# Optimization experiments

Hardware: AMD Instinct MI355X
Metric: run time of the kernel (lower is better)

The kernel has to match this reference:

```python
import jax, jax.numpy as jnp
import numpy as np

B, T, C = 2, 8192, 1024
H, BS, LW = 16, 64, 128          # num_heads, block_size, local_window_size
D = C // H                        # head_dim = 64
W = BS + LW                       # max window length per block = 192
NB = T // BS                      # number of blocks


def setup_inputs() -> dict:
    key = jax.random.key(0)
    ks = jax.random.split(key, 11)
    s = 1.0 / np.sqrt(C)          # small init so softmax is not saturated
    return {
        'query': jax.random.normal(ks[0], (B, T, C), jnp.float32),
        'key':   jax.random.normal(ks[1], (B, T, C), jnp.float32),
        'value': jax.random.normal(ks[2], (B, T, C), jnp.float32),
        'Wq': jax.random.normal(ks[3], (C, C), jnp.float32) * s,
        'bq': jax.random.normal(ks[4], (C,), jnp.float32) * s,
        'Wk': jax.random.normal(ks[5], (C, C), jnp.float32) * s,
        'bk': jax.random.normal(ks[6], (C,), jnp.float32) * s,
        'Wv': jax.random.normal(ks[7], (C, C), jnp.float32) * s,
        'bv': jax.random.normal(ks[8], (C,), jnp.float32) * s,
        'Wo': jax.random.normal(ks[9], (C, C), jnp.float32) * s,
        'bo': jax.random.normal(ks[10], (C,), jnp.float32) * s,
    }


def reference(query, key, value, Wq, bq, Wk, bk, Wv, bv, Wo, bo):
    # projections -> (B, H, T, D)
    def proj(x, Wt, bt):
        return (x @ Wt.T + bt).reshape(B, T, H, D).transpose(0, 2, 1, 3)

    scale = jnp.asarray(D, query.dtype) ** -0.5
    q = proj(query, Wq, bq) * scale
    k = proj(key, Wk, bk)
    v = proj(value, Wv, bv)

    # per-block window indices: block i attends to [i - LW//2, i + BS + LW//2)
    starts = jnp.arange(NB) * BS                              # (NB,)
    idx = starts[:, None] + jnp.arange(-LW // 2, BS + LW // 2)  # (NB, W)
    valid = (idx >= 0) & (idx < T)                            # (NB, W)
    cidx = jnp.clip(idx, 0, T - 1)

    q_blk = q.reshape(B, H, NB, BS, D)
    k_win = k[:, :, cidx, :]                                  # (B, H, NB, W, D)
    v_win = v[:, :, cidx, :]

    scores = jnp.einsum('bhnqd,bhnkd->bhnqk', q_blk, k_win).astype(jnp.float32)
    scores = jnp.where(valid[None, None, :, None, :], scores, -jnp.inf)
    probs = jax.nn.softmax(scores, axis=-1).astype(q.dtype)

    out = jnp.einsum('bhnqk,bhnkd->bhnqd', probs, v_win)      # (B, H, NB, BS, D)
    out = out.reshape(B, H, T, D).transpose(0, 2, 1, 3).reshape(B, T, C)
    return out @ Wo.T + bo
```

## Files before the change

### kernel.cpp

```cpp
#include <hip/hip_runtime.h>
#include <hip/hip_bf16.h>
#include <type_traits>

#define BATCH 2
#define SEQ   8192
#define CH    1024
#define NH    16
#define BLK   64
#define WIN   192
#define NBL   128
#define DH    64
#define MR    (BATCH*SEQ)

typedef __bf16 bf16x8 __attribute__((ext_vector_type(8)));
typedef float  f32x4  __attribute__((ext_vector_type(4)));

__device__ __forceinline__ f32x4 zero4() {
    f32x4 z; z[0]=0.f; z[1]=0.f; z[2]=0.f; z[3]=0.f; return z;
}

union Pack8 { __hip_bfloat16 h[8]; uint4 u; };

typedef const __attribute__((address_space(1))) unsigned int* gas_ptr;
typedef       __attribute__((address_space(3))) unsigned int* las_ptr;

__device__ __forceinline__ void gload_lds16(const __hip_bfloat16* g, __hip_bfloat16* l) {
    __builtin_amdgcn_global_load_lds((gas_ptr)(const void*)g, (las_ptr)(void*)l, 16, 0, 0);
}

__device__ __forceinline__ int xcd_swz(int bid, int nwg) {
    return (bid & 7) * (nwg >> 3) + (bid >> 3);
}

__global__ __launch_bounds__(256) void pack_bf16(
    const float* __restrict__ src, __hip_bfloat16* __restrict__ dst, int n8)
{
    int i = blockIdx.x * 256 + threadIdx.x;
    if (i >= n8) return;
    const float4* s = reinterpret_cast<const float4*>(src);
    float4 a = s[2 * i], b = s[2 * i + 1];
    Pack8 p;
    p.h[0] = __float2bfloat16(a.x); p.h[1] = __float2bfloat16(a.y);
    p.h[2] = __float2bfloat16(a.z); p.h[3] = __float2bfloat16(a.w);
    p.h[4] = __float2bfloat16(b.x); p.h[5] = __float2bfloat16(b.y);
    p.h[6] = __float2bfloat16(b.z); p.h[7] = __float2bfloat16(b.w);
    reinterpret_cast<uint4*>(dst)[i] = p.u;
}


__device__ __forceinline__ void stage_half(
    const __hip_bfloat16* __restrict__ g, int goff,
    __hip_bfloat16* sm, int loff, int tid)
{
    gload_lds16(g + goff,            sm + loff + tid * 8);
    gload_lds16(g + goff + 128 * CH, sm + loff + (tid + 512) * 8);
}

template<int MH, int KS>
__device__ __forceinline__ void phase_mfma(
    const __hip_bfloat16* As_, const __hip_bfloat16* Bs_,
    int aoff, int boff, f32x4 (&acc)[8][4])
{
    bf16x8 af[4], bf[4];
    #pragma unroll
    for (int i = 0; i < 4; ++i)
        af[i] = *reinterpret_cast<const bf16x8*>(As_ + KS * 8192 + (MH * 4 + i) * 512 + aoff);
    #pragma unroll
    for (int j = 0; j < 4; ++j)
        bf[j] = *reinterpret_cast<const bf16x8*>(Bs_ + KS * 8192 + j * 512 + boff);
    asm volatile("s_waitcnt lgkmcnt(0)" ::: "memory");
    __builtin_amdgcn_sched_barrier(0);
    __builtin_amdgcn_s_setprio(1);
    #pragma unroll
    for (int i = 0; i < 4; ++i)
        #pragma unroll
        for (int j = 0; j < 4; ++j)
            acc[MH * 4 + i][j] = __builtin_amdgcn_mfma_f32_16x16x32_bf16(
                af[i], bf[j], acc[MH * 4 + i][j], 0, 0, 0);
    __builtin_amdgcn_s_setprio(0);
}

template<typename OT>
__device__ __forceinline__ void gemm_body256(
    const __hip_bfloat16* __restrict__ A, const __hip_bfloat16* __restrict__ Wb,
    const float* __restrict__ bias, OT* __restrict__ out, float alpha,
    int m0, int n0, __hip_bfloat16* sm)
{
    const int tid  = threadIdx.x;
    const int wid  = tid >> 6;
    const int lane = tid & 63;
    const int quad = lane >> 4;
    const int l16  = lane & 15;
    const int wr   = wid >> 2, wc = wid & 3;

    const int r0 = tid >> 2;
    const int s0 = (tid & 3) ^ (r0 & 3);
    const int offA0 = (m0 + r0) * CH + s0 * 8;
    const int offB0 = (n0 + r0) * CH + s0 * 8;

    const int cq   = quad ^ (l16 & 3);
    const int aoff = ((wr * 128 + l16) * 4 + cq) * 8;
    const int boff = ((wc * 64  + l16) * 4 + cq) * 8;

    f32x4 acc[8][4];
    #pragma unroll
    for (int i = 0; i < 8; ++i)
        #pragma unroll
        for (int j = 0; j < 4; ++j) acc[i][j] = zero4();

    stage_half(A,  offA0,      sm, 0,             tid);
    stage_half(Wb, offB0,      sm, 32768,         tid);
    stage_half(A,  offA0 + 32, sm, 8192,          tid);
    stage_half(Wb, offB0 + 32, sm, 32768 + 8192,  tid);

    #pragma unroll 1
    for (int t = 0; t < 15; ++t) {
        const int cur = t & 1, nb = cur ^ 1;
        const int kn  = (t + 1) * 64;
        const __hip_bfloat16* As_ = sm + cur * 16384;
        const __hip_bfloat16* Bs_ = sm + 32768 + cur * 16384;

        asm volatile("s_waitcnt vmcnt(4)" ::: "memory");
        __builtin_amdgcn_s_barrier();
        __builtin_amdgcn_sched_barrier(0);
        stage_half(A, offA0 + kn, sm, nb * 16384, tid);
        phase_mfma<0, 0>(As_, Bs_, aoff, boff, acc);

        __builtin_amdgcn_s_barrier();
        __builtin_amdgcn_sched_barrier(0);
        stage_half(Wb, offB0 + kn, sm, 32768 + nb * 16384, tid);
        phase_mfma<1, 0>(As_, Bs_, aoff, boff, acc);

        asm volatile("s_waitcnt vmcnt(4)" ::: "memory");
        __builtin_amdgcn_s_barrier();
        __builtin_amdgcn_sched_barrier(0);
        stage_half(A, offA0 + kn + 32, sm, nb * 16384 + 8192, tid);
        phase_mfma<0, 1>(As_, Bs_, aoff, boff, acc);

        __builtin_amdgcn_s_barrier();
        __builtin_amdgcn_sched_barrier(0);
        stage_half(Wb, offB0 + kn + 32, sm, 32768 + nb * 16384 + 8192, tid);
        phase_mfma<1, 1>(As_, Bs_, aoff, boff, acc);
    }

    {
        const __hip_bfloat16* As_ = sm + 16384;
        const __hip_bfloat16* Bs_ = sm + 32768 + 16384;

        asm volatile("s_waitcnt vmcnt(4)" ::: "memory");
        __builtin_amdgcn_s_barrier();
        __builtin_amdgcn_sched_barrier(0);
        phase_mfma<0, 0>(As_, Bs_, aoff, boff, acc);

        __builtin_amdgcn_s_barrier();
        __builtin_amdgcn_sched_barrier(0);
        phase_mfma<1, 0>(As_, Bs_, aoff, boff, acc);

        asm volatile("s_waitcnt vmcnt(0)" ::: "memory");
        __builtin_amdgcn_s_barrier();
        __builtin_amdgcn_sched_barrier(0);
        phase_mfma<0, 1>(As_, Bs_, aoff, boff, acc);

        __builtin_amdgcn_s_barrier();
        __builtin_amdgcn_sched_barrier(0);
        phase_mfma<1, 1>(As_, Bs_, aoff, boff, acc);
    }

    #pragma unroll
    for (int j = 0; j < 4; ++j) {
        const int col = n0 + wc * 64 + j * 16 + l16;
        const float bv = bias[col];
        #pragma unroll
        for (int i = 0; i < 8; ++i) {
            #pragma unroll
            for (int r = 0; r < 4; ++r) {
                const int row = m0 + wr * 128 + i * 16 + quad * 4 + r;
                float v = alpha * (acc[i][j][r] + bv);
                if constexpr (std::is_same<OT, float>::value)
                    out[(size_t)row * CH + col] = v;
                else
                    out[(size_t)row * CH + col] = __float2bfloat16(v);
            }
        }
    }
}

__device__ __forceinline__ void gemm_tile256(int& m0, int& n0) {
    int bid = blockIdx.y * 4 + blockIdx.x;
    int swz = (bid & 7) * 32 + (bid >> 3);
    m0 = (swz >> 2) * 256;
    n0 = (swz & 3) * 256;
}

__global__ __launch_bounds__(512, 2) void gemm_qk256(
    const __hip_bfloat16* __restrict__ A0, const __hip_bfloat16* __restrict__ W0,
    const float* __restrict__ b0, __hip_bfloat16* __restrict__ o0, float alpha0,
    const __hip_bfloat16* __restrict__ A1, const __hip_bfloat16* __restrict__ W1,
    const float* __restrict__ b1, __hip_bfloat16* __restrict__ o1)
{
    __shared__ alignas(16) __hip_bfloat16 sm[65536];
    int m0, n0; gemm_tile256(m0, n0);
    if (blockIdx.z == 0)
        gemm_body256<__hip_bfloat16>(A0, W0, b0, o0, alpha0, m0, n0, sm);
    else
        gemm_body256<__hip_bfloat16>(A1, W1, b1, o1, 1.0f, m0, n0, sm);
}

template<typename OT>
__global__ __launch_bounds__(512, 2) void gemm_one256(
    const __hip_bfloat16* __restrict__ A, const __hip_bfloat16* __restrict__ Wb,
    const float* __restrict__ bias, OT* __restrict__ out)
{
    __shared__ alignas(16) __hip_bfloat16 sm[65536];
    int m0, n0; gemm_tile256(m0, n0);
    gemm_body256<OT>(A, Wb, bias, out, 1.0f, m0, n0, sm);
}

__global__ __launch_bounds__(256) void attn_kernel(
    const __hip_bfloat16* __restrict__ qg,
    const __hip_bfloat16* __restrict__ kg,
    const __hip_bfloat16* __restrict__ vg,
    __hip_bfloat16* __restrict__ ctx)
{
    __shared__ alignas(16) char smem[62464];
    auto qs = reinterpret_cast<__hip_bfloat16(*)[72]>(smem);
    auto ks = reinterpret_cast<__hip_bfloat16(*)[72]>(smem + 9216);
    auto vt = reinterpret_cast<__hip_bfloat16(*)[200]>(smem + 36864);
    auto ps = reinterpret_cast<__hip_bfloat16(*)[200]>(smem);

    const int blk = xcd_swz(blockIdx.x, BATCH * NH * NBL);
    const int n = blk & (NBL - 1);
    const int h = (blk >> 7) & (NH - 1);
    const int b = blk >> 11;
    const int t0  = n * BLK;
    const int kst = t0 - 64;
    const int tid = threadIdx.x;
    const size_t baseBH = (size_t)b * SEQ * CH + (size_t)h * DH;

    #pragma unroll
    for (int it = 0; it < 2; it++) {
        int c = tid + it * 256;
        int row = c >> 3, seg = c & 7;
        *reinterpret_cast<uint4*>(&qs[row][seg * 8]) =
            *reinterpret_cast<const uint4*>(qg + baseBH + (size_t)(t0 + row) * CH + seg * 8);
    }
    #pragma unroll
    for (int it = 0; it < 6; it++) {
        int c = tid + it * 256;
        int row = c >> 3, seg = c & 7;
        int tr = kst + row; tr = tr < 0 ? 0 : (tr >= SEQ ? SEQ - 1 : tr);
        *reinterpret_cast<uint4*>(&ks[row][seg * 8]) =
            *reinterpret_cast<const uint4*>(kg + baseBH + (size_t)tr * CH + seg * 8);
    }
    #pragma unroll
    for (int it = 0; it < 6; it++) {
        int c = tid + it * 256;
        int j = c % WIN, seg = c / WIN;
        int tr = kst + j; tr = tr < 0 ? 0 : (tr >= SEQ ? SEQ - 1 : tr);
        Pack8 p;
        p.u = *reinterpret_cast<const uint4*>(vg + baseBH + (size_t)tr * CH + seg * 8);
        #pragma unroll
        for (int e = 0; e < 8; e++) vt[seg * 8 + e][j] = p.h[e];
    }
    __syncthreads();

    const int wid = tid >> 6, lane = tid & 63, quad = lane >> 4, l16 = lane & 15;

    f32x4 sc[12];
    #pragma unroll
    for (int j = 0; j < 12; j++) sc[j] = zero4();
    #pragma unroll
    for (int kk = 0; kk < 2; kk++) {
        bf16x8 aq = *reinterpret_cast<const bf16x8*>(&qs[wid * 16 + l16][kk * 32 + quad * 8]);
        #pragma unroll
        for (int j = 0; j < 12; j++) {
            bf16x8 bk = *reinterpret_cast<const bf16x8*>(&ks[j * 16 + l16][kk * 32 + quad * 8]);
            sc[j] = __builtin_amdgcn_mfma_f32_16x16x32_bf16(aq, bk, sc[j], 0, 0, 0);
        }
    }
    __syncthreads();

    #pragma unroll
    for (int r = 0; r < 4; r++) {
        float s[12];
        float mx = -3.0e38f;
        #pragma unroll
        for (int j = 0; j < 12; j++) {
            int col = j * 16 + l16;
            int tr = kst + col;
            bool valid = (tr >= 0) && (tr < SEQ);
            s[j] = valid ? sc[j][r] : -3.0e38f;
            mx = fmaxf(mx, s[j]);
        }
        #pragma unroll
        for (int o = 1; o < 16; o <<= 1) mx = fmaxf(mx, __shfl_xor(mx, o, 64));
        float sum = 0.f;
        #pragma unroll
        for (int j = 0; j < 12; j++) {
            float e = __expf(s[j] - mx);
            s[j] = e;
            sum += e;
        }
        #pragma unroll
        for (int o = 1; o < 16; o <<= 1) sum += __shfl_xor(sum, o, 64);
        const float inv = 1.f / sum;
        const int row = wid * 16 + quad * 4 + r;
        #pragma unroll
        for (int j = 0; j < 12; j++)
            ps[row][j * 16 + l16] = __float2bfloat16(s[j] * inv);
    }
    __syncthreads();

    f32x4 oa[4];
    #pragma unroll
    for (int j = 0; j < 4; j++) oa[j] = zero4();
    #pragma unroll
    for (int kk = 0; kk < 6; kk++) {
        bf16x8 ap = *reinterpret_cast<const bf16x8*>(&ps[wid * 16 + l16][kk * 32 + quad * 8]);
        #pragma unroll
        for (int j = 0; j < 4; j++) {
            bf16x8 bv = *reinterpret_cast<const bf16x8*>(&vt[j * 16 + l16][kk * 32 + quad * 8]);
            oa[j] = __builtin_amdgcn_mfma_f32_16x16x32_bf16(ap, bv, oa[j], 0, 0, 0);
        }
    }
    #pragma unroll
    for (int j = 0; j < 4; j++) {
        const int d = j * 16 + l16;
        #pragma unroll
        for (int r = 0; r < 4; r++) {
            const int i = wid * 16 + quad * 4 + r;
            ctx[baseBH + (size_t)(t0 + i) * CH + d] = __float2bfloat16(oa[j][r]);
        }
    }
}

extern "C" void kernel_launch(void* const* d_in, const int* in_sizes, int n_in,
                              void* d_out, int out_size, void* d_ws, size_t ws_size,
                              hipStream_t stream)
{
    const float* query = (const float*)d_in[0];
    const float* key_i = (const float*)d_in[1];
    const float* value = (const float*)d_in[2];
    const float* Wq = (const float*)d_in[3];
    const float* bq = (const float*)d_in[4];
    const float* Wk = (const float*)d_in[5];
    const float* bk = (const float*)d_in[6];
    const float* Wv = (const float*)d_in[7];
    const float* bv = (const float*)d_in[8];
    const float* Wo = (const float*)d_in[9];
    const float* bo = (const float*)d_in[10];
    float* out = (float*)d_out;

    const size_t NELEM = (size_t)MR * CH;
    const size_t WELEM = (size_t)CH * CH;

    __hip_bfloat16* S0 = (__hip_bfloat16*)d_ws;
    __hip_bfloat16* S1 = S0 + NELEM;
    __hip_bfloat16* S2 = S1 + NELEM;
    __hip_bfloat16* S3 = S2 + NELEM;
    __hip_bfloat16* wqb = S3;
    __hip_bfloat16* wkb = S3 + WELEM;
    __hip_bfloat16* wvb = S3 + 2 * WELEM;
    __hip_bfloat16* wob = S3 + 3 * WELEM;

    __hip_bfloat16* xq = (__hip_bfloat16*)d_out;
    __hip_bfloat16* xk = xq + NELEM;
    __hip_bfloat16* vb = (__hip_bfloat16*)d_out;
    __hip_bfloat16* qb = S1;
    __hip_bfloat16* kb = S2;
    __hip_bfloat16* cb = S0;

    const int nA8 = (int)(NELEM / 8);
    const int nW8 = (int)(WELEM / 8);

    pack_bf16<<<nA8 / 256, 256, 0, stream>>>(query, xq, nA8);
    pack_bf16<<<nA8 / 256, 256, 0, stream>>>(key_i, xk, nA8);
    pack_bf16<<<nA8 / 256, 256, 0, stream>>>(value, S0, nA8);
    pack_bf16<<<nW8 / 256, 256, 0, stream>>>(Wq, wqb, nW8);
    pack_bf16<<<nW8 / 256, 256, 0, stream>>>(Wk, wkb, nW8);
    pack_bf16<<<nW8 / 256, 256, 0, stream>>>(Wv, wvb, nW8);
    pack_bf16<<<nW8 / 256, 256, 0, stream>>>(Wo, wob, nW8);

    dim3 ggrid(CH / 256, MR / 256);
    dim3 qkgrid(CH / 256, MR / 256, 2);

    gemm_qk256<<<qkgrid, 512, 0, stream>>>(xq, wqb, bq, qb, 0.125f,
                                           xk, wkb, bk, kb);
    gemm_one256<__hip_bfloat16><<<ggrid, 512, 0, stream>>>(S0, wvb, bv, vb);

    attn_kernel<<<BATCH * NH * NBL, 256, 0, stream>>>(qb, kb, vb, cb);

    gemm_one256<float><<<ggrid, 512, 0, stream>>>(cb, wob, bo, out);
}
```

Baseline: 451.8 us.

## Merge GEMM phases, interleave LDS fragment loads with MFMAs, change LDS swizzle

The projection GEMM's four half-phases per K-step become two. Each phase now issues both the A and B global-to-LDS loads, then runs all 8x4 MFMAs, which halves the number of workgroup barriers. Within a phase, A fragments are loaded from LDS in a rolling fashion with partial lgkmcnt waits, so MFMAs start before every fragment arrives. The LDS XOR swizzle now uses row bits 1-2 instead of bits 0-1, to reduce bank conflicts on fragment reads. This adds register pressure from keeping all B fragments plus rotating A fragments live, and issues the loads in larger bursts.

```diff
diff --git a/kernel.cpp b/kernel.cpp
--- a/kernel.cpp
+++ b/kernel.cpp
@@ -56,27 +56,44 @@
     gload_lds16(g + goff + 128 * CH, sm + loff + (tid + 512) * 8);
 }
 
-template<int MH, int KS>
-__device__ __forceinline__ void phase_mfma(
+#define SB0 __builtin_amdgcn_sched_barrier(0)
+#define LGKM(n) do { asm volatile("s_waitcnt lgkmcnt(" #n ")" ::: "memory"); \
+                     __builtin_amdgcn_sched_barrier(0); } while (0)
+#define MFMA4(i, areg) do { \
+    acc[i][0] = __builtin_amdgcn_mfma_f32_16x16x32_bf16(areg, bf0, acc[i][0], 0, 0, 0); \
+    acc[i][1] = __builtin_amdgcn_mfma_f32_16x16x32_bf16(areg, bf1, acc[i][1], 0, 0, 0); \
+    acc[i][2] = __builtin_amdgcn_mfma_f32_16x16x32_bf16(areg, bf2, acc[i][2], 0, 0, 0); \
+    acc[i][3] = __builtin_amdgcn_mfma_f32_16x16x32_bf16(areg, bf3, acc[i][3], 0, 0, 0); } while (0)
+
+template<int KS>
+__device__ __forceinline__ void phase_mfma2(
     const __hip_bfloat16* As_, const __hip_bfloat16* Bs_,
     int aoff, int boff, f32x4 (&acc)[8][4])
 {
-    bf16x8 af[4], bf[4];
-    #pragma unroll
-    for (int i = 0; i < 4; ++i)
-        af[i] = *reinterpret_cast<const bf16x8*>(As_ + KS * 8192 + (MH * 4 + i) * 512 + aoff);
-    #pragma unroll
-    for (int j = 0; j < 4; ++j)
-        bf[j] = *reinterpret_cast<const bf16x8*>(Bs_ + KS * 8192 + j * 512 + boff);
-    asm volatile("s_waitcnt lgkmcnt(0)" ::: "memory");
-    __builtin_amdgcn_sched_barrier(0);
+    const __hip_bfloat16* Ak = As_ + KS * 8192;
+    const __hip_bfloat16* Bk = Bs_ + KS * 8192;
+    bf16x8 bf0 = *reinterpret_cast<const bf16x8*>(Bk + boff);
+    bf16x8 bf1 = *reinterpret_cast<const bf16x8*>(Bk + boff + 512);
+    bf16x8 bf2 = *reinterpret_cast<const bf16x8*>(Bk + boff + 1024);
+    bf16x8 bf3 = *reinterpret_cast<const bf16x8*>(Bk + boff + 1536);
+    bf16x8 a0  = *reinterpret_cast<const bf16x8*>(Ak + aoff);
+    bf16x8 a1  = *reinterpret_cast<const bf16x8*>(Ak + aoff + 512);
+    bf16x8 a2  = *reinterpret_cast<const bf16x8*>(Ak + aoff + 1024);
+    SB0;
     __builtin_amdgcn_s_setprio(1);
-    #pragma unroll
-    for (int i = 0; i < 4; ++i)
-        #pragma unroll
-        for (int j = 0; j < 4; ++j)
-            acc[MH * 4 + i][j] = __builtin_amdgcn_mfma_f32_16x16x32_bf16(
-                af[i], bf[j], acc[MH * 4 + i][j], 0, 0, 0);
+    LGKM(2);  MFMA4(0, a0);
+    bf16x8 a3 = *reinterpret_cast<const bf16x8*>(Ak + aoff + 3 * 512); SB0;
+    LGKM(2);  MFMA4(1, a1);
+    a0 = *reinterpret_cast<const bf16x8*>(Ak + aoff + 4 * 512); SB0;
+    LGKM(2);  MFMA4(2, a2);
+    a1 = *reinterpret_cast<const bf16x8*>(Ak + aoff + 5 * 512); SB0;
+    LGKM(2);  MFMA4(3, a3);
+    a2 = *reinterpret_cast<const bf16x8*>(Ak + aoff + 6 * 512); SB0;
+    LGKM(2);  MFMA4(4, a0);
+    a3 = *reinterpret_cast<const bf16x8*>(Ak + aoff + 7 * 512); SB0;
+    LGKM(2);  MFMA4(5, a1);
+    LGKM(1);  MFMA4(6, a2);
+    LGKM(0);  MFMA4(7, a3);
     __builtin_amdgcn_s_setprio(0);
 }
 
@@ -94,11 +111,11 @@
     const int wr   = wid >> 2, wc = wid & 3;
 
     const int r0 = tid >> 2;
-    const int s0 = (tid & 3) ^ (r0 & 3);
+    const int s0 = (tid & 3) ^ ((tid >> 3) & 3);
     const int offA0 = (m0 + r0) * CH + s0 * 8;
     const int offB0 = (n0 + r0) * CH + s0 * 8;
 
-    const int cq   = quad ^ (l16 & 3);
+    const int cq   = quad ^ ((l16 >> 1) & 3);
     const int aoff = ((wr * 128 + l16) * 4 + cq) * 8;
     const int boff = ((wc * 64  + l16) * 4 + cq) * 8;
 
@@ -122,25 +139,17 @@
 
         asm volatile("s_waitcnt vmcnt(4)" ::: "memory");
         __builtin_amdgcn_s_barrier();
-        __builtin_amdgcn_sched_barrier(0);
-        stage_half(A, offA0 + kn, sm, nb * 16384, tid);
-        phase_mfma<0, 0>(As_, Bs_, aoff, boff, acc);
-
-        __builtin_amdgcn_s_barrier();
-        __builtin_amdgcn_sched_barrier(0);
+        SB0;
+        stage_half(A,  offA0 + kn, sm, nb * 16384, tid);
         stage_half(Wb, offB0 + kn, sm, 32768 + nb * 16384, tid);
-        phase_mfma<1, 0>(As_, Bs_, aoff, boff, acc);
+        phase_mfma2<0>(As_, Bs_, aoff, boff, acc);
 
         asm volatile("s_waitcnt vmcnt(4)" ::: "memory");
         __builtin_amdgcn_s_barrier();
-        __builtin_amdgcn_sched_barrier(0);
-        stage_half(A, offA0 + kn + 32, sm, nb * 16384 + 8192, tid);
-        phase_mfma<0, 1>(As_, Bs_, aoff, boff, acc);
-
-        __builtin_amdgcn_s_barrier();
-        __builtin_amdgcn_sched_barrier(0);
+        SB0;
+        stage_half(A,  offA0 + kn + 32, sm, nb * 16384 + 8192, tid);
         stage_half(Wb, offB0 + kn + 32, sm, 32768 + nb * 16384 + 8192, tid);
-        phase_mfma<1, 1>(As_, Bs_, aoff, boff, acc);
+        phase_mfma2<1>(As_, Bs_, aoff, boff, acc);
     }
 
     {
@@ -149,21 +158,13 @@
 
         asm volatile("s_waitcnt vmcnt(4)" ::: "memory");
         __builtin_amdgcn_s_barrier();
-        __builtin_amdgcn_sched_barrier(0);
-        phase_mfma<0, 0>(As_, Bs_, aoff, boff, acc);
-
-        __builtin_amdgcn_s_barrier();
-        __builtin_amdgcn_sched_barrier(0);
-        phase_mfma<1, 0>(As_, Bs_, aoff, boff, acc);
+        SB0;
+        phase_mfma2<0>(As_, Bs_, aoff, boff, acc);
 
         asm volatile("s_waitcnt vmcnt(0)" ::: "memory");
         __builtin_amdgcn_s_barrier();
-        __builtin_amdgcn_sched_barrier(0);
-        phase_mfma<0, 1>(As_, Bs_, aoff, boff, acc);
-
-        __builtin_amdgcn_s_barrier();
-        __builtin_amdgcn_sched_barrier(0);
-        phase_mfma<1, 1>(As_, Bs_, aoff, boff, acc);
+        SB0;
+        phase_mfma2<1>(As_, Bs_, aoff, boff, acc);
     }
 
     #pragma unroll
```

Result: no change. 447.6 us (-0.9%).

## Reorder GEMM LDS reads before global stages, reuse B fragments, change LDS swizzle

Applied to the files above, without the earlier changes.

Restructures the 256-tile GEMM main loop so each phase issues its LDS fragment reads before the next global-to-LDS stage, then waits at a barrier and runs the MFMAs. B fragments are loaded once per K-slice and reused across both M halves, which cuts redundant LDS reads. The XOR swizzle now uses bits 1-2 of the row instead of bits 0-1, aimed at fewer LDS bank conflicts. The barrier and vmcnt placement changes the hazard ordering between LDS reads and async writes, which could cost correctness or add stalls if the ordering is wrong.

```diff
diff --git a/kernel.cpp b/kernel.cpp
--- a/kernel.cpp
+++ b/kernel.cpp
@@ -56,27 +56,38 @@
     gload_lds16(g + goff + 128 * CH, sm + loff + (tid + 512) * 8);
 }
 
-template<int MH, int KS>
-__device__ __forceinline__ void phase_mfma(
-    const __hip_bfloat16* As_, const __hip_bfloat16* Bs_,
-    int aoff, int boff, f32x4 (&acc)[8][4])
-{
-    bf16x8 af[4], bf[4];
+#define SB0 __builtin_amdgcn_sched_barrier(0)
+#define LGKM0 do { asm volatile("s_waitcnt lgkmcnt(0)" ::: "memory"); \
+                   __builtin_amdgcn_sched_barrier(0); } while (0)
+#define VMCNT(n) do { asm volatile("s_waitcnt vmcnt(" #n ")" ::: "memory"); \
+                      __builtin_amdgcn_sched_barrier(0); } while (0)
+
+template<int MH, bool RB>
+__device__ __forceinline__ void phase_reads(
+    const __hip_bfloat16* Ak, const __hip_bfloat16* Bk,
+    int aoff, int boff, bf16x8 (&af)[4], bf16x8 (&bfk)[4])
+{
+    if constexpr (RB) {
+        #pragma unroll
+        for (int j = 0; j < 4; ++j)
+            bfk[j] = *reinterpret_cast<const bf16x8*>(Bk + boff + j * 512);
+    }
     #pragma unroll
     for (int i = 0; i < 4; ++i)
-        af[i] = *reinterpret_cast<const bf16x8*>(As_ + KS * 8192 + (MH * 4 + i) * 512 + aoff);
-    #pragma unroll
-    for (int j = 0; j < 4; ++j)
-        bf[j] = *reinterpret_cast<const bf16x8*>(Bs_ + KS * 8192 + j * 512 + boff);
-    asm volatile("s_waitcnt lgkmcnt(0)" ::: "memory");
-    __builtin_amdgcn_sched_barrier(0);
+        af[i] = *reinterpret_cast<const bf16x8*>(Ak + aoff + (MH * 4 + i) * 512);
+}
+
+template<int MH>
+__device__ __forceinline__ void phase_mfma16(
+    const bf16x8 (&af)[4], const bf16x8 (&bfk)[4], f32x4 (&acc)[8][4])
+{
     __builtin_amdgcn_s_setprio(1);
     #pragma unroll
     for (int i = 0; i < 4; ++i)
         #pragma unroll
         for (int j = 0; j < 4; ++j)
             acc[MH * 4 + i][j] = __builtin_amdgcn_mfma_f32_16x16x32_bf16(
-                af[i], bf[j], acc[MH * 4 + i][j], 0, 0, 0);
+                af[i], bfk[j], acc[MH * 4 + i][j], 0, 0, 0);
     __builtin_amdgcn_s_setprio(0);
 }
 
@@ -94,11 +105,11 @@
     const int wr   = wid >> 2, wc = wid & 3;
 
     const int r0 = tid >> 2;
-    const int s0 = (tid & 3) ^ (r0 & 3);
+    const int s0 = (tid & 3) ^ ((tid >> 3) & 3);
     const int offA0 = (m0 + r0) * CH + s0 * 8;
     const int offB0 = (n0 + r0) * CH + s0 * 8;
 
-    const int cq   = quad ^ (l16 & 3);
+    const int cq   = quad ^ ((l16 >> 1) & 3);
     const int aoff = ((wr * 128 + l16) * 4 + cq) * 8;
     const int boff = ((wc * 64  + l16) * 4 + cq) * 8;
 
@@ -112,6 +123,11 @@
     stage_half(Wb, offB0,      sm, 32768,         tid);
     stage_half(A,  offA0 + 32, sm, 8192,          tid);
     stage_half(Wb, offB0 + 32, sm, 32768 + 8192,  tid);
+    VMCNT(4);
+    __builtin_amdgcn_s_barrier();
+    SB0;
+
+    bf16x8 af[4], bfk[4];
 
     #pragma unroll 1
     for (int t = 0; t < 15; ++t) {
@@ -120,50 +136,72 @@
         const __hip_bfloat16* As_ = sm + cur * 16384;
         const __hip_bfloat16* Bs_ = sm + 32768 + cur * 16384;
 
-        asm volatile("s_waitcnt vmcnt(4)" ::: "memory");
-        __builtin_amdgcn_s_barrier();
-        __builtin_amdgcn_sched_barrier(0);
+        phase_reads<0, true>(As_, Bs_, aoff, boff, af, bfk);
         stage_half(A, offA0 + kn, sm, nb * 16384, tid);
-        phase_mfma<0, 0>(As_, Bs_, aoff, boff, acc);
-
-        __builtin_amdgcn_s_barrier();
-        __builtin_amdgcn_sched_barrier(0);
+        SB0;
+        __builtin_amdgcn_s_barrier();
+        LGKM0;
+        phase_mfma16<0>(af, bfk, acc);
+        __builtin_amdgcn_s_barrier();
+
+        phase_reads<1, false>(As_, Bs_, aoff, boff, af, bfk);
         stage_half(Wb, offB0 + kn, sm, 32768 + nb * 16384, tid);
-        phase_mfma<1, 0>(As_, Bs_, aoff, boff, acc);
-
-        asm volatile("s_waitcnt vmcnt(4)" ::: "memory");
-        __builtin_amdgcn_s_barrier();
-        __builtin_amdgcn_sched_barrier(0);
+        SB0;
+        __builtin_amdgcn_s_barrier();
+        LGKM0;
+        phase_mfma16<1>(af, bfk, acc);
+        VMCNT(4);
+        __builtin_amdgcn_s_barrier();
+
+        phase_reads<0, true>(As_ + 8192, Bs_ + 8192, aoff, boff, af, bfk);
         stage_half(A, offA0 + kn + 32, sm, nb * 16384 + 8192, tid);
-        phase_mfma<0, 1>(As_, Bs_, aoff, boff, acc);
-
-        __builtin_amdgcn_s_barrier();
-        __builtin_amdgcn_sched_barrier(0);
+        SB0;
+        __builtin_amdgcn_s_barrier();
+        LGKM0;
+        phase_mfma16<0>(af, bfk, acc);
+        __builtin_amdgcn_s_barrier();
+
+        phase_reads<1, false>(As_ + 8192, Bs_ + 8192, aoff, boff, af, bfk);
         stage_half(Wb, offB0 + kn + 32, sm, 32768 + nb * 16384 + 8192, tid);
-        phase_mfma<1, 1>(As_, Bs_, aoff, boff, acc);
+        SB0;
+        __builtin_amdgcn_s_barrier();
+        LGKM0;
+        phase_mfma16<1>(af, bfk, acc);
+        VMCNT(4);
+        __builtin_amdgcn_s_barrier();
     }
 
     {
         const __hip_bfloat16* As_ = sm + 16384;
         const __hip_bfloat16* Bs_ = sm + 32768 + 16384;
 
-        asm volatile("s_waitcnt vmcnt(4)" ::: "memory");
-        __builtin_amdgcn_s_barrier();
-        __builtin_amdgcn_sched_barrier(0);
-        phase_mfma<0, 0>(As_, Bs_, aoff, boff, acc);
-
-        __builtin_amdgcn_s_barrier();
-        __builtin_amdgcn_sched_barrier(0);
-        phase_mfma<1, 0>(As_, Bs_, aoff, boff, acc);
-
-        asm volatile("s_waitcnt vmcnt(0)" ::: "memory");
-        __builtin_amdgcn_s_barrier();
-        __builtin_amdgcn_sched_barrier(0);
-        phase_mfma<0, 1>(As_, Bs_, aoff, boff, acc);
-
-        __builtin_amdgcn_s_barrier();
-        __builtin_amdgcn_sched_barrier(0);
-        phase_mfma<1, 1>(As_, Bs_, aoff, boff, acc);
+        phase_reads<0, true>(As_, Bs_, aoff, boff, af, bfk);
+        SB0;
+        __builtin_amdgcn_s_barrier();
+        LGKM0;
+        phase_mfma16<0>(af, bfk, acc);
+        __builtin_amdgcn_s_barrier();
+
+        phase_reads<1, false>(As_, Bs_, aoff, boff, af, bfk);
+        SB0;
+        __builtin_amdgcn_s_barrier();
+        LGKM0;
+        phase_mfma16<1>(af, bfk, acc);
+        VMCNT(0);
+        __builtin_amdgcn_s_barrier();
+
+        phase_reads<0, true>(As_ + 8192, Bs_ + 8192, aoff, boff, af, bfk);
+        SB0;
+        __builtin_amdgcn_s_barrier();
+        LGKM0;
+        phase_mfma16<0>(af, bfk, acc);
+        __builtin_amdgcn_s_barrier();
+
+        phase_reads<1, false>(As_ + 8192, Bs_ + 8192, aoff, boff, af, bfk);
+        SB0;
+        __builtin_amdgcn_s_barrier();
+        LGKM0;
+        phase_mfma16<1>(af, bfk, acc);
     }
 
     #pragma unroll
```

Result: no change. 448.8 us (-0.7%).
